# Kernel tuning notes

Hardware: AMD Instinct MI355X
Metric: run time of the kernel (lower is better)

The kernel has to match this reference:

```python
import jax, jax.numpy as jnp
import numpy as np

ALPHA = 1.702
LIMIT = 7.0


def setup_inputs() -> dict:
    key = jax.random.key(0)
    ks = jax.random.split(key, 6)
    T, H, D, E = 8192, 1024, 1024, 8
    hidden_states = jax.random.normal(ks[0], (T, H), dtype=jnp.float32)
    routing_weights = jax.random.uniform(ks[1], (T, E), dtype=jnp.float32)
    # 0.02 scale keeps activations in a sane range (original uses raw randn params)
    gate_up_proj = jax.random.normal(ks[2], (E, H, 2 * D), dtype=jnp.float32) * 0.02
    gate_up_proj_bias = jax.random.normal(ks[3], (E, 2 * D), dtype=jnp.float32) * 0.02
    down_proj = jax.random.normal(ks[4], (E, D, H), dtype=jnp.float32) * 0.02
    down_proj_bias = jax.random.normal(ks[5], (E, H), dtype=jnp.float32) * 0.02
    return {
        "hidden_states": hidden_states,
        "routing_weights": routing_weights,
        "gate_up_proj": gate_up_proj,
        "gate_up_proj_bias": gate_up_proj_bias,
        "down_proj": down_proj,
        "down_proj_bias": down_proj_bias,
    }


def reference(hidden_states, routing_weights, gate_up_proj, gate_up_proj_bias,
              down_proj, down_proj_bias):
    # hidden_states: [T, H]; routing_weights: [T, E] (batch_size == T in the torch code)
    B, H = hidden_states.shape[0], hidden_states.shape[-1]
    hs = hidden_states.reshape(-1, H)  # [T, H]
    # all-experts batched GEMM: [E, T, 2D]
    gate_up = jnp.einsum('th,ehd->etd', hs, gate_up_proj) + gate_up_proj_bias[:, None, :]
    gate = jnp.minimum(gate_up[..., ::2], LIMIT)          # [E, T, D]
    up = jnp.clip(gate_up[..., 1::2], -LIMIT, LIMIT)      # [E, T, D]
    glu = gate * jax.nn.sigmoid(gate * ALPHA)
    # down projection: [E, T, H]
    next_states = jnp.einsum('etd,edh->eth', (up + 1.0) * glu, down_proj) \
        + down_proj_bias[:, None, :]
    # routing-weighted combine over experts: [T, H]
    out = jnp.einsum('eth,te->th', next_states, routing_weights)
    return out.reshape(B, -1, H)  # [T, 1, H], matching final .view(batch_size, -1, hidden)
```

## Files before the change

kernel.cpp:

```cpp
#include <hip/hip_runtime.h>
#include <hip/hip_bf16.h>

#define T_DIM 8192
#define H_DIM 1024
#define D_DIM 1024
#define E_DIM 8
#define TWO_D 2048
#define K2 8192

#define ALPHA_C 1.702f
#define LIMIT_C 7.0f

typedef __attribute__((ext_vector_type(8))) short s8v;
typedef __attribute__((ext_vector_type(4))) float f4v;

__device__ __forceinline__ void g2l16(const void* g, void* l) {
    __builtin_amdgcn_global_load_lds((const __attribute__((address_space(1))) void*)g,
                                     (__attribute__((address_space(3))) void*)l, 16, 0, 0);
}

__device__ __forceinline__ unsigned short f2bf(float f) {
    __hip_bfloat16 h = __float2bfloat16(f);
    return __builtin_bit_cast(unsigned short, h);
}

__device__ __forceinline__ float bf2f(unsigned short u) {
    unsigned int x = ((unsigned int)u) << 16;
    return __builtin_bit_cast(float, x);
}


__global__ void f32_to_bf16_kernel(const float* __restrict__ in,
                                   unsigned short* __restrict__ out, size_t n) {
    size_t i = ((size_t)blockIdx.x * blockDim.x + threadIdx.x) * 4;
    if (i + 3 < n) {
        float4 v = *(const float4*)(in + i);
        ushort4 o;
        o.x = f2bf(v.x); o.y = f2bf(v.y); o.z = f2bf(v.z); o.w = f2bf(v.w);
        *(ushort4*)(out + i) = o;
    }
}

__global__ void transpose_conv_kernel(const float* __restrict__ in,
                                      unsigned short* __restrict__ out,
                                      int cols, size_t ibs, size_t obs, size_t ors,
                                      int remap) {
    __shared__ float t[32][33];
    const int b = blockIdx.z;
    const int c0 = blockIdx.x * 32, r0 = blockIdx.y * 32;
    const int tx = threadIdx.x & 31, ty = threadIdx.x >> 5;
    const float* ip = in + (size_t)b * ibs;
    #pragma unroll
    for (int i = 0; i < 4; ++i)
        t[ty + i * 8][tx] = ip[(size_t)(r0 + ty + i * 8) * cols + c0 + tx];
    __syncthreads();
    unsigned short* op = out + (size_t)b * obs;
    #pragma unroll
    for (int i = 0; i < 4; ++i) {
        int c = c0 + ty + i * 8;
        int nc = remap ? ((c & ~31) + ((c & 1) << 4) + ((c >> 1) & 15)) : c;
        op[(size_t)nc * ors + r0 + tx] = f2bf(t[tx][ty + i * 8]);
    }
}

__global__ void reduce_bias_kernel(const unsigned short* __restrict__ p0,
                                   const float* __restrict__ rw,
                                   const float* __restrict__ b3,
                                   float* __restrict__ out) {
    const int t = blockIdx.x;
    const int h = threadIdx.x * 4;
    const size_t idx = (size_t)t * H_DIM + h;
    float r[E_DIM];
    #pragma unroll
    for (int e = 0; e < E_DIM; ++e) r[e] = rw[(size_t)t * E_DIM + e];
    float4 v = *(const float4*)(out + idx);
    ushort4 a = *(const ushort4*)(p0 + idx);
    v.x += bf2f(a.x);
    v.y += bf2f(a.y);
    v.z += bf2f(a.z);
    v.w += bf2f(a.w);
    #pragma unroll
    for (int e = 0; e < E_DIM; ++e) {
        float4 bb = *(const float4*)(b3 + (size_t)e * H_DIM + h);
        v.x += r[e] * bb.x; v.y += r[e] * bb.y; v.z += r[e] * bb.z; v.w += r[e] * bb.w;
    }
    *(float4*)(out + idx) = v;
}


#define FEN asm volatile("" ::: "memory")
#define BARR { FEN; __builtin_amdgcn_s_barrier(); FEN; }
#define LGKM0 asm volatile("s_waitcnt lgkmcnt(0)" ::: "memory")

#define LDA4(BUF, KH, CH)                                                        \
  { const short* _p = &As[BUF][KH][aoff + (CH) * 2048];                          \
    a[0] = *(const s8v*)(_p);        a[1] = *(const s8v*)(_p + 512);             \
    a[2] = *(const s8v*)(_p + 1024); a[3] = *(const s8v*)(_p + 1536); }

#define LDB4(BUF, KH)                                                            \
  { const short* _p = &Bs[BUF][KH][boff];                                        \
    b[0] = *(const s8v*)(_p);        b[1] = *(const s8v*)(_p + 512);             \
    b[2] = *(const s8v*)(_p + 1024); b[3] = *(const s8v*)(_p + 1536); }

#define MM16(CH)                                                                 \
  { _Pragma("unroll")                                                            \
    for (int mf = 0; mf < 4; ++mf) {                                             \
      _Pragma("unroll")                                                          \
      for (int nf = 0; nf < 4; ++nf)                                             \
        acc[(CH) * 4 + mf][nf] = __builtin_amdgcn_mfma_f32_16x16x32_bf16(        \
            a[mf], b[nf], acc[(CH) * 4 + mf][nf], 0, 0, 0);                      \
    } }

#define STG(GB, SLOT, KEL)                                                       \
  { const short* _g = (GB) + (size_t)rstage * sK + (KEL) + gco;                  \
    g2l16(_g, &(SLOT)[wave * 1024]);                                             \
    g2l16(_g + 16 * sK, &(SLOT)[wave * 1024 + 512]); }

#define PHASE_TAIL(CH)                                                           \
  BARR; LGKM0;                                                                   \
  __builtin_amdgcn_s_setprio(1);                                                 \
  MM16(CH);                                                                      \
  __builtin_amdgcn_s_setprio(0);                                                 \
  BARR;

#define TILE(T, BUF)                                                             \
  { const int _kel = kbase + (T) * 64;                                           \
    LDA4(BUF, 0, 0); LDB4(BUF, 0);                                               \
    if ((T) + 1 < NT) STG(Ag, As[(BUF) ^ 1][1], _kel + 96);                      \
    PHASE_TAIL(0)                                                                \
    LDA4(BUF, 0, 1);                                                             \
    if ((T) + 1 < NT) STG(Bg, Bs[(BUF) ^ 1][1], _kel + 96);                      \
    PHASE_TAIL(1)                                                                \
    LDA4(BUF, 1, 0); LDB4(BUF, 1);                                               \
    if ((T) + 2 < NT) STG(Ag, As[BUF][0], _kel + 128);                           \
    PHASE_TAIL(0)                                                                \
    LDA4(BUF, 1, 1);                                                             \
    if ((T) + 2 < NT) STG(Bg, Bs[BUF][0], _kel + 128);                           \
    if ((T) + 2 < NT) { asm volatile("s_waitcnt vmcnt(4)" ::: "memory"); }       \
    else              { asm volatile("s_waitcnt vmcnt(0)" ::: "memory"); }       \
    PHASE_TAIL(1)                                                                \
  }

__device__ __forceinline__ void gemm_core(const short* __restrict__ Ag,
                                          const short* __restrict__ Bg,
                                          const size_t sK, const int kbase,
                                          const int NT, f4v (&acc)[8][4]) {
    __shared__ __align__(16) short As[2][2][8192];
    __shared__ __align__(16) short Bs[2][2][8192];
    const int tid = threadIdx.x;
    const int lane = tid & 63;
    const int wave = tid >> 6;
    const int wm = wave >> 2, wn = wave & 3;
    const int cq = lane & 15, quad = lane >> 4;
    const int gco = (((lane & 3) ^ ((lane >> 3) & 3)) << 3);
    const int rstage = wave * 32 + (lane >> 2);
    const int rc = ((quad ^ ((cq >> 1) & 3)) << 3);
    const int aoff = wm * 4096 + cq * 32 + rc;
    const int boff = wn * 2048 + cq * 32 + rc;

    s8v a[4], b[4];
    #pragma unroll
    for (int i = 0; i < 8; ++i)
        #pragma unroll
        for (int j = 0; j < 4; ++j) acc[i][j] = (f4v){0.f, 0.f, 0.f, 0.f};

    STG(Ag, As[0][0], kbase);
    STG(Bg, Bs[0][0], kbase);
    STG(Ag, As[0][1], kbase + 32);
    STG(Bg, Bs[0][1], kbase + 32);
    STG(Ag, As[1][0], kbase + 64);
    STG(Bg, Bs[1][0], kbase + 64);
    asm volatile("s_waitcnt vmcnt(4)" ::: "memory");
    BARR;

    #pragma unroll 1
    for (int t = 0; t < NT; t += 2) {
        TILE(t, 0)
        TILE(t + 1, 1)
    }
}


__global__ __launch_bounds__(512, 2) void gemm1_kernel(
    const short* __restrict__ Ag0,
    const short* __restrict__ Bg0,
    const float* __restrict__ b1,
    const float* __restrict__ rw,
    __hip_bfloat16* __restrict__ act2)
{
    const int e = blockIdx.z;
    const int mBase = blockIdx.x * 256;
    const int nBase = blockIdx.y * 256;
    const short* Ag = Ag0 + (size_t)mBase * H_DIM;
    const short* Bg = Bg0 + ((size_t)e * TWO_D + nBase) * H_DIM;

    f4v acc[8][4];
    gemm_core(Ag, Bg, H_DIM, 0, H_DIM / 64, acc);

    const int lane = threadIdx.x & 63, wave = threadIdx.x >> 6;
    const int wm = wave >> 2, wn = wave & 3;
    const int cq = lane & 15, quad = lane >> 4;

    #pragma unroll
    for (int p = 0; p < 2; ++p) {
        const int j = (((nBase + wn * 64 + p * 32) >> 5) << 4) + cq;
        const float gb = b1[(size_t)e * TWO_D + 2 * j];
        const float ub = b1[(size_t)e * TWO_D + 2 * j + 1];
        #pragma unroll
        for (int fm = 0; fm < 8; ++fm) {
            #pragma unroll
            for (int r = 0; r < 4; ++r) {
                const int row = mBase + wm * 128 + fm * 16 + quad * 4 + r;
                const float rwv = rw[(size_t)row * E_DIM + e];
                float gate = acc[fm][2 * p][r] + gb;
                float up   = acc[fm][2 * p + 1][r] + ub;
                gate = fminf(gate, LIMIT_C);
                up = fminf(fmaxf(up, -LIMIT_C), LIMIT_C);
                float glu = gate / (1.f + __expf(-ALPHA_C * gate));
                float av = (up + 1.f) * glu * rwv;
                act2[(size_t)row * K2 + (size_t)e * D_DIM + j] = __float2bfloat16(av);
            }
        }
    }
}


__global__ __launch_bounds__(512, 2) void gemm2_kernel(
    const short* __restrict__ Ag0,
    const short* __restrict__ Bg0,
    float* __restrict__ out,
    unsigned short* __restrict__ p0)
{
    const int id = blockIdx.x;
    const int nBase = (id & 3) * 256;
    const int mBase = ((id >> 2) & 31) * 256;
    const int kIdx = id >> 7;
    const short* Ag = Ag0 + (size_t)mBase * K2;
    const short* Bg = Bg0 + (size_t)nBase * K2;

    f4v acc[8][4];
    gemm_core(Ag, Bg, K2, kIdx * 4096, 4096 / 64, acc);

    const int lane = threadIdx.x & 63, wave = threadIdx.x >> 6;
    const int wm = wave >> 2, wn = wave & 3;
    const int cq = lane & 15, quad = lane >> 4;

    #pragma unroll
    for (int fm = 0; fm < 8; ++fm) {
        #pragma unroll
        for (int r = 0; r < 4; ++r) {
            const int row = mBase + wm * 128 + fm * 16 + quad * 4 + r;
            #pragma unroll
            for (int nf = 0; nf < 4; ++nf) {
                const size_t o = (size_t)row * H_DIM + nBase + wn * 64 + nf * 16 + cq;
                if (kIdx == 0) out[o] = acc[fm][nf][r];
                else           p0[o]  = f2bf(acc[fm][nf][r]);
            }
        }
    }
}


extern "C" void kernel_launch(void* const* d_in, const int* in_sizes, int n_in,
                              void* d_out, int out_size, void* d_ws, size_t ws_size,
                              hipStream_t stream) {
    const float* hs = (const float*)d_in[0];
    const float* rw = (const float*)d_in[1];
    const float* w1 = (const float*)d_in[2];
    const float* b1 = (const float*)d_in[3];
    const float* w3 = (const float*)d_in[4];
    const float* b3 = (const float*)d_in[5];
    float* out = (float*)d_out;

    char* ws = (char*)d_ws;
    unsigned short* hsb  = (unsigned short*)(ws);
    unsigned short* w1b  = (unsigned short*)(ws + ((size_t)16 << 20));
    unsigned short* w3b  = (unsigned short*)(ws + ((size_t)48 << 20));
    unsigned short* act2 = (unsigned short*)(ws + ((size_t)64 << 20));
    unsigned short* p0 = (unsigned short*)(ws);

    {
        size_t n = (size_t)T_DIM * H_DIM;
        f32_to_bf16_kernel<<<dim3(n / (256 * 4)), dim3(256), 0, stream>>>(hs, hsb, n);
    }
    transpose_conv_kernel<<<dim3(TWO_D / 32, H_DIM / 32, E_DIM), dim3(256), 0, stream>>>(
        w1, w1b, TWO_D, (size_t)H_DIM * TWO_D, (size_t)TWO_D * H_DIM, (size_t)H_DIM, 1);
    transpose_conv_kernel<<<dim3(H_DIM / 32, D_DIM / 32, E_DIM), dim3(256), 0, stream>>>(
        w3, w3b, H_DIM, (size_t)D_DIM * H_DIM, (size_t)D_DIM, (size_t)K2, 0);
    gemm1_kernel<<<dim3(T_DIM / 256, TWO_D / 256, E_DIM), dim3(512), 0, stream>>>(
        (const short*)hsb, (const short*)w1b, b1, rw, (__hip_bfloat16*)act2);
    gemm2_kernel<<<dim3(256), dim3(512), 0, stream>>>(
        (const short*)act2, (const short*)w3b, out, p0);
    reduce_bias_kernel<<<dim3(T_DIM), dim3(H_DIM / 4), 0, stream>>>(
        p0, rw, b3, out);
}
```

Before: 638.8 us.

## Restructure GEMM LDS staging into full-K64 tiles with 8-way swizzle and double buffer

Changes the shared-memory layout from two 32-wide K halves per buffer to a single 64-wide K row per tile with an 8-way XOR swizzle, and reorganises the prefetch schedule so that each tile's next-tile loads are issued in four chunks across the MMA phases with vmcnt(2) waits. This is meant to cut LDS bank conflicts and make global-to-LDS prefetch overlap more evenly with MFMA work. It also adds sched_barrier after the lgkm waits to pin instruction ordering. The prefetch depth drops from about 1.5 tiles ahead to one tile ahead, which risks exposing more global memory latency.

```diff
diff --git a/kernel.cpp b/kernel.cpp
--- a/kernel.cpp
+++ b/kernel.cpp
@@ -90,17 +90,20 @@
 
 #define FEN asm volatile("" ::: "memory")
 #define BARR { FEN; __builtin_amdgcn_s_barrier(); FEN; }
-#define LGKM0 asm volatile("s_waitcnt lgkmcnt(0)" ::: "memory")
-
-#define LDA4(BUF, KH, CH)                                                        \
-  { const short* _p = &As[BUF][KH][aoff + (CH) * 2048];                          \
-    a[0] = *(const s8v*)(_p);        a[1] = *(const s8v*)(_p + 512);             \
-    a[2] = *(const s8v*)(_p + 1024); a[3] = *(const s8v*)(_p + 1536); }
-
-#define LDB4(BUF, KH)                                                            \
-  { const short* _p = &Bs[BUF][KH][boff];                                        \
-    b[0] = *(const s8v*)(_p);        b[1] = *(const s8v*)(_p + 512);             \
-    b[2] = *(const s8v*)(_p + 1024); b[3] = *(const s8v*)(_p + 1536); }
+#define LGKM0 { asm volatile("s_waitcnt lgkmcnt(0)" ::: "memory"); \
+                __builtin_amdgcn_sched_barrier(0); }
+#define VMW2 asm volatile("s_waitcnt vmcnt(2)" ::: "memory")
+#define VMW0 asm volatile("s_waitcnt vmcnt(0)" ::: "memory")
+
+#define LDA4(BUF, KS, CH)                                                        \
+  { const short* _p = &As[BUF][awm + (CH) * 4096 + ((KS) ? rc1 : rc0)];          \
+    a[0] = *(const s8v*)(_p);        a[1] = *(const s8v*)(_p + 1024);            \
+    a[2] = *(const s8v*)(_p + 2048); a[3] = *(const s8v*)(_p + 3072); }
+
+#define LDB4(BUF, KS)                                                            \
+  { const short* _p = &Bs[BUF][bwn + ((KS) ? rc1 : rc0)];                        \
+    b[0] = *(const s8v*)(_p);        b[1] = *(const s8v*)(_p + 1024);            \
+    b[2] = *(const s8v*)(_p + 2048); b[3] = *(const s8v*)(_p + 3072); }
 
 #define MM16(CH)                                                                 \
   { _Pragma("unroll")                                                            \
@@ -111,52 +114,60 @@
             a[mf], b[nf], acc[(CH) * 4 + mf][nf], 0, 0, 0);                      \
     } }
 
-#define STG(GB, SLOT, KEL)                                                       \
-  { const short* _g = (GB) + (size_t)rstage * sK + (KEL) + gco;                  \
-    g2l16(_g, &(SLOT)[wave * 1024]);                                             \
-    g2l16(_g + 16 * sK, &(SLOT)[wave * 1024 + 512]); }
-
-#define PHASE_TAIL(CH)                                                           \
-  BARR; LGKM0;                                                                   \
-  __builtin_amdgcn_s_setprio(1);                                                 \
-  MM16(CH);                                                                      \
-  __builtin_amdgcn_s_setprio(0);                                                 \
-  BARR;
+#define STG_A(BUF, CH, KEL)                                                      \
+  { const int _rb = (wave >> 2) * 128 + (wave & 3) * 16 + (CH) * 64;             \
+    const short* _g = Ag + (size_t)(_rb + rloc) * sK + (KEL) + gco;              \
+    short* _d = &As[BUF][_rb * 64];                                              \
+    g2l16(_g, _d); g2l16(_g + 8 * sK, _d + 512); }
+
+#define STG_B(BUF, HALF, KEL)                                                    \
+  { const int _rb = (HALF) * 128 + wave * 16;                                    \
+    const short* _g = Bg + (size_t)(_rb + rloc) * sK + (KEL) + gco;              \
+    short* _d = &Bs[BUF][_rb * 64];                                              \
+    g2l16(_g, _d); g2l16(_g + 8 * sK, _d + 512); }
+
+#define PRIO_MM(CH) { __builtin_amdgcn_s_setprio(1); MM16(CH);                   \
+                      __builtin_amdgcn_s_setprio(0); }
 
 #define TILE(T, BUF)                                                             \
-  { const int _kel = kbase + (T) * 64;                                           \
+  { const int _kel = kbase + ((T) + 1) * 64;                                     \
+    const bool _pf = (T) + 1 < NT;                                               \
     LDA4(BUF, 0, 0); LDB4(BUF, 0);                                               \
-    if ((T) + 1 < NT) STG(Ag, As[(BUF) ^ 1][1], _kel + 96);                      \
-    PHASE_TAIL(0)                                                                \
+    if (_pf) STG_A((BUF) ^ 1, 0, _kel);                                          \
+    BARR; LGKM0; PRIO_MM(0);                                                     \
+    if (_pf) { VMW2; } else { VMW0; }                                            \
+    BARR;                                                                        \
     LDA4(BUF, 0, 1);                                                             \
-    if ((T) + 1 < NT) STG(Bg, Bs[(BUF) ^ 1][1], _kel + 96);                      \
-    PHASE_TAIL(1)                                                                \
+    if (_pf) STG_B((BUF) ^ 1, 0, _kel);                                          \
+    BARR; LGKM0; PRIO_MM(1); BARR;                                               \
     LDA4(BUF, 1, 0); LDB4(BUF, 1);                                               \
-    if ((T) + 2 < NT) STG(Ag, As[BUF][0], _kel + 128);                           \
-    PHASE_TAIL(0)                                                                \
+    if (_pf) STG_B((BUF) ^ 1, 1, _kel);                                          \
+    BARR; LGKM0; PRIO_MM(0); BARR;                                               \
     LDA4(BUF, 1, 1);                                                             \
-    if ((T) + 2 < NT) STG(Bg, Bs[BUF][0], _kel + 128);                           \
-    if ((T) + 2 < NT) { asm volatile("s_waitcnt vmcnt(4)" ::: "memory"); }       \
-    else              { asm volatile("s_waitcnt vmcnt(0)" ::: "memory"); }       \
-    PHASE_TAIL(1)                                                                \
+    if (_pf) STG_A((BUF) ^ 1, 1, _kel);                                          \
+    BARR; LGKM0; PRIO_MM(1);                                                     \
+    if (_pf) { VMW2; } else { VMW0; }                                            \
+    BARR;                                                                        \
   }
 
 __device__ __forceinline__ void gemm_core(const short* __restrict__ Ag,
                                           const short* __restrict__ Bg,
                                           const size_t sK, const int kbase,
                                           const int NT, f4v (&acc)[8][4]) {
-    __shared__ __align__(16) short As[2][2][8192];
-    __shared__ __align__(16) short Bs[2][2][8192];
+    __shared__ __align__(16) short As[2][16384];
+    __shared__ __align__(16) short Bs[2][16384];
     const int tid = threadIdx.x;
     const int lane = tid & 63;
     const int wave = tid >> 6;
     const int wm = wave >> 2, wn = wave & 3;
     const int cq = lane & 15, quad = lane >> 4;
-    const int gco = (((lane & 3) ^ ((lane >> 3) & 3)) << 3);
-    const int rstage = wave * 32 + (lane >> 2);
-    const int rc = ((quad ^ ((cq >> 1) & 3)) << 3);
-    const int aoff = wm * 4096 + cq * 32 + rc;
-    const int boff = wn * 2048 + cq * 32 + rc;
+    const int cq7 = cq & 7;
+    const int rloc = lane >> 3;
+    const int gco = (((lane & 7) ^ rloc)) * 8;
+    const int awm = wm * 8192 + cq * 64;
+    const int bwn = wn * 4096 + cq * 64;
+    const int rc0 = (quad ^ cq7) * 8;
+    const int rc1 = ((quad + 4) ^ cq7) * 8;
 
     s8v a[4], b[4];
     #pragma unroll
@@ -164,13 +175,11 @@
         #pragma unroll
         for (int j = 0; j < 4; ++j) acc[i][j] = (f4v){0.f, 0.f, 0.f, 0.f};
 
-    STG(Ag, As[0][0], kbase);
-    STG(Bg, Bs[0][0], kbase);
-    STG(Ag, As[0][1], kbase + 32);
-    STG(Bg, Bs[0][1], kbase + 32);
-    STG(Ag, As[1][0], kbase + 64);
-    STG(Bg, Bs[1][0], kbase + 64);
-    asm volatile("s_waitcnt vmcnt(4)" ::: "memory");
+    STG_A(0, 0, kbase);
+    STG_B(0, 0, kbase);
+    STG_B(0, 1, kbase);
+    STG_A(0, 1, kbase);
+    VMW2;
     BARR;
 
     #pragma unroll 1
```

Result: faster. 625.3 us (-2.1%).
